# Kernel optimization log

Measured on AMD Instinct MI355X. Metric: run time of the kernel, lower is better.

Reference implementation:

```python
import jax, jax.numpy as jnp
import numpy as np

N = 8192
IN_F = 256
OUT_F = 64
ALPHA = 0.2
NEG_INF = -9e15


def setup_inputs() -> dict:
    key = jax.random.key(0)
    k1, k2, k3, k4 = jax.random.split(key, 4)
    h = jax.random.normal(k1, (N, IN_F), dtype=jnp.float32)
    W = jax.random.normal(k2, (IN_F, OUT_F), dtype=jnp.float32) * (1.414 / np.sqrt(IN_F))
    a = jax.random.normal(k3, (2 * OUT_F, 1), dtype=jnp.float32) * (1.414 / np.sqrt(2 * OUT_F))
    adj = jax.random.randint(k4, (N, N), 0, 2, dtype=jnp.int32)
    return {"h": h, "W": W, "a": a, "adj": adj}


def reference(h, W, a, adj):
    # Wh: [N, F]
    Wh = h @ W
    # Decompose concat-based attention: e_ij = LeakyReLU(Wh_i . a[:F] + Wh_j . a[F:])
    a1, a2 = a[:OUT_F], a[OUT_F:]
    src = Wh @ a1              # [N, 1] contribution of row i
    dst = Wh @ a2              # [N, 1] contribution of col j
    e = jax.nn.leaky_relu(src + dst.T, negative_slope=ALPHA)  # [N, N]
    e = jnp.where(adj > 0, e, NEG_INF)
    attention = jax.nn.softmax(e, axis=1)
    # dropout is identity in eval mode
    h_prime = attention @ Wh   # [N, F]
    return h_prime
```

## Files before the change

### kernel.cpp

```cpp
#include <hip/hip_runtime.h>

#define NROWS 8192
#define NSPLIT 8
#define JT (NROWS / NSPLIT)
#define NITER (JT / 64)
#define L2E 1.4426950408889634f

typedef __attribute__((ext_vector_type(4))) float f32x4;
typedef __attribute__((ext_vector_type(8))) __bf16 bf16x8;
typedef __attribute__((ext_vector_type(4))) unsigned int u32x4;

__device__ __forceinline__ unsigned short f2bf(float x) {
  unsigned u = __float_as_uint(x);
  u += 0x7fffu + ((u >> 16) & 1u);
  return (unsigned short)(u >> 16);
}

__global__ __launch_bounds__(256) void k_prep(
    const float* __restrict__ h, const float* __restrict__ W,
    const float* __restrict__ a, unsigned short* __restrict__ WhB,
    float* __restrict__ src, float* __restrict__ dst) {
  int i = blockIdx.x * 4 + (threadIdx.x >> 6);
  int lane = threadIdx.x & 63;
  const float* hrow = h + (size_t)i * 256;
  float s = 0.f;
#pragma unroll 4
  for (int k = 0; k < 256; k += 4) {
    float4 hv = *(const float4*)(hrow + k);
    s = fmaf(hv.x, W[(k + 0) * 64 + lane], s);
    s = fmaf(hv.y, W[(k + 1) * 64 + lane], s);
    s = fmaf(hv.z, W[(k + 2) * 64 + lane], s);
    s = fmaf(hv.w, W[(k + 3) * 64 + lane], s);
  }
  int nt = lane >> 4, c = lane & 15;
  int gi = (i >> 3) & 3, e = i & 7;
  int idx = ((((i >> 5) * 4 + nt) * 64) + c + 16 * gi) * 8 + e;
  WhB[idx] = f2bf(s);
  float v1 = s * a[lane];
  float v2 = s * a[64 + lane];
#pragma unroll
  for (int d = 32; d; d >>= 1) {
    v1 += __shfl_xor(v1, d);
    v2 += __shfl_xor(v2, d);
  }
  if (lane == 0) {
    src[i] = v1 * L2E;
    dst[i] = v2 * L2E;
  }
}

__global__ __launch_bounds__(256) void k_dmax(
    const float* __restrict__ dst, float* __restrict__ dmax) {
  __shared__ float red[4];
  float v = -INFINITY;
  for (int i = threadIdx.x; i < NROWS; i += 256) v = fmaxf(v, dst[i]);
#pragma unroll
  for (int d = 32; d; d >>= 1) v = fmaxf(v, __shfl_xor(v, d));
  if ((threadIdx.x & 63) == 0) red[threadIdx.x >> 6] = v;
  __syncthreads();
  if (threadIdx.x == 0)
    *dmax = fmaxf(fmaxf(red[0], red[1]), fmaxf(red[2], red[3]));
}

__global__ __launch_bounds__(256) void k_pack(
    const int* __restrict__ adj, unsigned long long* __restrict__ packed) {
  int row = blockIdx.x * 4 + (threadIdx.x >> 6);
  int lane = threadIdx.x & 63;
  const int* rp = adj + (size_t)row * NROWS;
#pragma unroll
  for (int half = 0; half < 2; ++half) {
    unsigned long long word = 0;
#pragma unroll 8
    for (int it = 0; it < 64; ++it) {
      int v = rp[half * 4096 + it * 64 + lane];
      unsigned long long bal = __ballot(v > 0);
      word = (lane == it) ? bal : word;
    }
    packed[(size_t)row * 128 + half * 64 + lane] = word;
  }
}

__global__ __launch_bounds__(256, 4) void k_attn(
    const unsigned long long* __restrict__ packed,
    const unsigned short* __restrict__ WhB,
    const float* __restrict__ src, const float* __restrict__ dst,
    const float* __restrict__ dmax,
    float* __restrict__ pl, float* __restrict__ pacc) {
  __shared__ float ldst[JT];
  int task = blockIdx.x * 4 + (threadIdx.x >> 6);
  int sp = task >> 9;
  int mt = task & 511;
  int lane = threadIdx.x & 63;
  int r = lane & 15;
  int g = lane >> 4;
  int row0 = mt * 16;
  int jbase = sp * JT;

  for (int k = threadIdx.x; k < JT; k += 256) ldst[k] = dst[jbase + k];
  __syncthreads();

  float srcr = src[row0 + r];
  float vB = srcr + *dmax;
  float Mi = fmaxf(vB, 0.2f * vB);

  float lrow = 0.f;
  f32x4 acc[4] = {f32x4{0.f, 0.f, 0.f, 0.f}, f32x4{0.f, 0.f, 0.f, 0.f},
                  f32x4{0.f, 0.f, 0.f, 0.f}, f32x4{0.f, 0.f, 0.f, 0.f}};
  const unsigned long long* pwp =
      packed + (size_t)(row0 + r) * (NROWS / 64) + (jbase >> 6);
  const bf16x8* Bfr = (const bf16x8*)WhB;

#pragma unroll
  for (int it = 0; it < NITER; ++it) {
    const int jb = it * 64;

    unsigned long long pw = pwp[it];

    int jc = (jbase + jb) >> 5;
    const bf16x8* bp = Bfr + (size_t)jc * 256 + lane;
    bf16x8 b0 = bp[0];
    bf16x8 b1 = bp[64];
    bf16x8 b2 = bp[128];
    bf16x8 b3 = bp[192];
    bf16x8 b4 = bp[256];
    bf16x8 b5 = bp[320];
    bf16x8 b6 = bp[384];
    bf16x8 b7 = bp[448];

    const float* dl = ldst + jb + 8 * g;
    float4 d0 = *(const float4*)(dl);
    float4 d1 = *(const float4*)(dl + 4);
    float4 d2 = *(const float4*)(dl + 32);
    float4 d3 = *(const float4*)(dl + 36);

    unsigned lo = (unsigned)(pw >> (8 * g));
    unsigned hi = (unsigned)(pw >> (32 + 8 * g));

    float p[16];
#define PE(P, BIT, DD)                    \
  {                                       \
    float v_ = srcr + (DD);               \
    v_ = fmaxf(v_, 0.2f * v_);            \
    float e_ = exp2f(v_ - Mi);            \
    (P) = (BIT) ? e_ : 0.f;               \
  }
    PE(p[0], lo & 1u, d0.x)   PE(p[1], lo & 2u, d0.y)
    PE(p[2], lo & 4u, d0.z)   PE(p[3], lo & 8u, d0.w)
    PE(p[4], lo & 16u, d1.x)  PE(p[5], lo & 32u, d1.y)
    PE(p[6], lo & 64u, d1.z)  PE(p[7], lo & 128u, d1.w)
    PE(p[8], hi & 1u, d2.x)   PE(p[9], hi & 2u, d2.y)
    PE(p[10], hi & 4u, d2.z)  PE(p[11], hi & 8u, d2.w)
    PE(p[12], hi & 16u, d3.x) PE(p[13], hi & 32u, d3.y)
    PE(p[14], hi & 64u, d3.z) PE(p[15], hi & 128u, d3.w)
#undef PE

    unsigned q[8];
#pragma unroll
    for (int t = 0; t < 16; t += 2) {
      lrow += p[t] + p[t + 1];
      unsigned qq;
      asm("v_cvt_pk_bf16_f32 %0, %1, %2" : "=v"(qq) : "v"(p[t]), "v"(p[t + 1]));
      q[t >> 1] = qq;
    }
    u32x4 qv0 = {q[0], q[1], q[2], q[3]};
    u32x4 qv1 = {q[4], q[5], q[6], q[7]};
    bf16x8 A0 = __builtin_bit_cast(bf16x8, qv0);
    bf16x8 A1 = __builtin_bit_cast(bf16x8, qv1);

    __builtin_amdgcn_s_setprio(1);
    acc[0] = __builtin_amdgcn_mfma_f32_16x16x32_bf16(A0, b0, acc[0], 0, 0, 0);
    acc[1] = __builtin_amdgcn_mfma_f32_16x16x32_bf16(A0, b1, acc[1], 0, 0, 0);
    acc[2] = __builtin_amdgcn_mfma_f32_16x16x32_bf16(A0, b2, acc[2], 0, 0, 0);
    acc[3] = __builtin_amdgcn_mfma_f32_16x16x32_bf16(A0, b3, acc[3], 0, 0, 0);
    acc[0] = __builtin_amdgcn_mfma_f32_16x16x32_bf16(A1, b4, acc[0], 0, 0, 0);
    acc[1] = __builtin_amdgcn_mfma_f32_16x16x32_bf16(A1, b5, acc[1], 0, 0, 0);
    acc[2] = __builtin_amdgcn_mfma_f32_16x16x32_bf16(A1, b6, acc[2], 0, 0, 0);
    acc[3] = __builtin_amdgcn_mfma_f32_16x16x32_bf16(A1, b7, acc[3], 0, 0, 0);
    __builtin_amdgcn_s_setprio(0);
  }

  lrow += __shfl_xor(lrow, 16);
  lrow += __shfl_xor(lrow, 32);
  if (lane < 16) pl[sp * NROWS + row0 + lane] = lrow;
#pragma unroll
  for (int nt = 0; nt < 4; nt++)
#pragma unroll
    for (int q2 = 0; q2 < 4; q2++)
      pacc[((size_t)sp * NROWS + row0 + 4 * g + q2) * 64 + nt * 16 + r] = acc[nt][q2];
}

__global__ __launch_bounds__(256) void k_comb(
    const float* __restrict__ pl, const float* __restrict__ pacc,
    float* __restrict__ out) {
  int t = blockIdx.x * 256 + threadIdx.x;
  int row = t >> 6, f = t & 63;
  float L = 0.f, o = 0.f;
#pragma unroll
  for (int s2 = 0; s2 < NSPLIT; s2++) {
    L += pl[s2 * NROWS + row];
    o += pacc[((size_t)s2 * NROWS + row) * 64 + f];
  }
  out[t] = o / L;
}

extern "C" void kernel_launch(void* const* d_in, const int* in_sizes, int n_in,
                              void* d_out, int out_size, void* d_ws, size_t ws_size,
                              hipStream_t stream) {
  const float* h = (const float*)d_in[0];
  const float* W = (const float*)d_in[1];
  const float* a = (const float*)d_in[2];
  const int* adj = (const int*)d_in[3];
  float* out = (float*)d_out;

  char* ws = (char*)d_ws;
  unsigned short* WhB = (unsigned short*)ws;
  float* src = (float*)(ws + 0x100000);
  float* dst = (float*)(ws + 0x108000);
  float* dmax = (float*)(ws + 0x110000);
  float* pl = (float*)(ws + 0x110100);
  float* pacc = (float*)(ws + 0x150100);
  unsigned long long* packed = (unsigned long long*)(ws + 0x1150100);

  hipLaunchKernelGGL(k_prep, dim3(NROWS / 4), dim3(256), 0, stream, h, W, a, WhB, src, dst);
  hipLaunchKernelGGL(k_dmax, dim3(1), dim3(256), 0, stream, dst, dmax);
  hipLaunchKernelGGL(k_pack, dim3(NROWS / 4), dim3(256), 0, stream, adj, packed);
  hipLaunchKernelGGL(k_attn, dim3(512 * NSPLIT / 4), dim3(256), 0, stream,
                     packed, WhB, src, dst, dmax, pl, pacc);
  hipLaunchKernelGGL(k_comb, dim3(NROWS * 64 / 256), dim3(256), 0, stream, pl, pacc, out);
}
```

Before: 131.5 us.

## Fuse adjacency bit-packing into attention kernel via in-register ballots

Removes the separate k_pack kernel and its packed-mask round trip through global memory. Each attention wave now reads its 16x1024 int adjacency tile, builds 64-bit masks with ballots, stores them in four registers spread across lanes, and broadcasts them with shuffles inside the main loop. This saves one launch and the write and re-read of the packed mask. In exchange, the 256 MB adj read now happens in a prologue before the MFMA loop, with no overlap against compute inside each wave, and it adds register pressure.

```diff
diff --git a/kernel.cpp b/kernel.cpp
--- a/kernel.cpp
+++ b/kernel.cpp
@@ -62,27 +62,8 @@
     *dmax = fmaxf(fmaxf(red[0], red[1]), fmaxf(red[2], red[3]));
 }
 
-__global__ __launch_bounds__(256) void k_pack(
-    const int* __restrict__ adj, unsigned long long* __restrict__ packed) {
-  int row = blockIdx.x * 4 + (threadIdx.x >> 6);
-  int lane = threadIdx.x & 63;
-  const int* rp = adj + (size_t)row * NROWS;
-#pragma unroll
-  for (int half = 0; half < 2; ++half) {
-    unsigned long long word = 0;
-#pragma unroll 8
-    for (int it = 0; it < 64; ++it) {
-      int v = rp[half * 4096 + it * 64 + lane];
-      unsigned long long bal = __ballot(v > 0);
-      word = (lane == it) ? bal : word;
-    }
-    packed[(size_t)row * 128 + half * 64 + lane] = word;
-  }
-}
-
 __global__ __launch_bounds__(256, 4) void k_attn(
-    const unsigned long long* __restrict__ packed,
-    const unsigned short* __restrict__ WhB,
+    const int* __restrict__ adj, const unsigned short* __restrict__ WhB,
     const float* __restrict__ src, const float* __restrict__ dst,
     const float* __restrict__ dmax,
     float* __restrict__ pl, float* __restrict__ pacc) {
@@ -99,6 +80,25 @@
   for (int k = threadIdx.x; k < JT; k += 256) ldst[k] = dst[jbase + k];
   __syncthreads();
 
+  unsigned long long mk0 = 0, mk1 = 0, mk2 = 0, mk3 = 0;
+  {
+    const int* abase = adj + (size_t)row0 * NROWS + jbase + lane;
+#pragma unroll
+    for (int rr = 0; rr < 16; ++rr) {
+      const int* rp = abase + (size_t)rr * NROWS;
+#pragma unroll
+      for (int ch = 0; ch < 16; ++ch) {
+        int v = rp[ch * 64];
+        unsigned long long bal = __ballot(v > 0);
+        const int holder = ((ch & 3) << 4) + rr;
+        if ((ch >> 2) == 0) mk0 = (lane == holder) ? bal : mk0;
+        if ((ch >> 2) == 1) mk1 = (lane == holder) ? bal : mk1;
+        if ((ch >> 2) == 2) mk2 = (lane == holder) ? bal : mk2;
+        if ((ch >> 2) == 3) mk3 = (lane == holder) ? bal : mk3;
+      }
+    }
+  }
+
   float srcr = src[row0 + r];
   float vB = srcr + *dmax;
   float Mi = fmaxf(vB, 0.2f * vB);
@@ -106,15 +106,17 @@
   float lrow = 0.f;
   f32x4 acc[4] = {f32x4{0.f, 0.f, 0.f, 0.f}, f32x4{0.f, 0.f, 0.f, 0.f},
                   f32x4{0.f, 0.f, 0.f, 0.f}, f32x4{0.f, 0.f, 0.f, 0.f}};
-  const unsigned long long* pwp =
-      packed + (size_t)(row0 + r) * (NROWS / 64) + (jbase >> 6);
   const bf16x8* Bfr = (const bf16x8*)WhB;
 
 #pragma unroll
   for (int it = 0; it < NITER; ++it) {
     const int jb = it * 64;
 
-    unsigned long long pw = pwp[it];
+    unsigned long long pw;
+    if ((it >> 2) == 0) pw = __shfl(mk0, ((it & 3) << 4) + r);
+    if ((it >> 2) == 1) pw = __shfl(mk1, ((it & 3) << 4) + r);
+    if ((it >> 2) == 2) pw = __shfl(mk2, ((it & 3) << 4) + r);
+    if ((it >> 2) == 3) pw = __shfl(mk3, ((it & 3) << 4) + r);
 
     int jc = (jbase + jb) >> 5;
     const bf16x8* bp = Bfr + (size_t)jc * 256 + lane;
@@ -219,12 +221,10 @@
   float* dmax = (float*)(ws + 0x110000);
   float* pl = (float*)(ws + 0x110100);
   float* pacc = (float*)(ws + 0x150100);
-  unsigned long long* packed = (unsigned long long*)(ws + 0x1150100);
 
   hipLaunchKernelGGL(k_prep, dim3(NROWS / 4), dim3(256), 0, stream, h, W, a, WhB, src, dst);
   hipLaunchKernelGGL(k_dmax, dim3(1), dim3(256), 0, stream, dst, dmax);
-  hipLaunchKernelGGL(k_pack, dim3(NROWS / 4), dim3(256), 0, stream, adj, packed);
   hipLaunchKernelGGL(k_attn, dim3(512 * NSPLIT / 4), dim3(256), 0, stream,
-                     packed, WhB, src, dst, dmax, pl, pacc);
+                     adj, WhB, src, dst, dmax, pl, pacc);
   hipLaunchKernelGGL(k_comb, dim3(NROWS * 64 / 256), dim3(256), 0, stream, pl, pacc, out);
 }
```

New measurement: 118.3 us. 1.11x faster.
